# Optimization experiments

Hardware: AMD Instinct MI355X
Metric: run time of the kernel (lower is better)

## Reference

```python
import jax, jax.numpy as jnp
import numpy as np

TOKENS, IN_F, OUT_F = 16384, 4096, 4096
Q_MAX_I8 = 127.0


def setup_inputs() -> dict:
    key = jax.random.key(0)
    k1, k2, k3, k4 = jax.random.split(key, 4)
    x = jax.random.normal(k1, (TOKENS, IN_F), dtype=jnp.float32)
    # packed int4 weights: two nibbles per byte along dim=1 -> [out, in//2]
    qweight = jax.random.randint(k2, (OUT_F, IN_F // 2), 0, 256, dtype=jnp.int32)
    # per-output-channel symmetric scale (positive)
    weight_scale = jax.random.uniform(k3, (OUT_F, 1), dtype=jnp.float32) * 0.01 + 1e-4
    bias = jax.random.normal(k4, (OUT_F,), dtype=jnp.float32)
    return {"x": x, "qweight": qweight, "weight_scale": weight_scale, "bias": bias}


def _unpack_int4(qweight):
    # high nibble -> even columns, low nibble -> odd columns (pack dim=1)
    high = (qweight >> 4) - 8            # [out, in//2], values in [-8, 7]
    low = (qweight & 15) - 8
    out_f = qweight.shape[0]
    return jnp.stack([high, low], axis=-1).reshape(out_f, -1)  # [out, in]


def reference(x, qweight, weight_scale, bias):
    # dequantize int4 weight: per-output-channel symmetric scale
    w = _unpack_int4(qweight).astype(jnp.float32) * weight_scale  # [out, in]
    # dynamic per-sample symmetric int8 activation fake-quant
    max_abs = jnp.max(jnp.abs(x), axis=-1, keepdims=True)         # [tokens, 1]
    act_scale = max_abs / Q_MAX_I8
    act_scale = jnp.where(act_scale == 0, 1.0, act_scale)
    q_x = jnp.clip(jnp.round(x / act_scale), -128.0, 127.0)
    x_dq = q_x * act_scale
    return x_dq @ w.T + bias
```

## Files before the change

### kernel.cpp

```cpp
#include <hip/hip_runtime.h>
#include <cstdint>

#define TOKENS 16384
#define IN_F   4096
#define OUT_F  4096

typedef int v4i __attribute__((ext_vector_type(4)));

__device__ __forceinline__ void async_lds16(const void* g, const void* l) {
    __builtin_amdgcn_global_load_lds(
        (const __attribute__((address_space(1))) void*)(uintptr_t)g,
        (__attribute__((address_space(3))) void*)(uint32_t)(uintptr_t)l,
        16, 0, 0);
}

__global__ __launch_bounds__(256) void act_quant_kernel(
        const float* __restrict__ x,
        signed char* __restrict__ qx,
        float* __restrict__ act_scale) {
    const int row = blockIdx.x;
    const int tid = threadIdx.x;
    const float4* xr = (const float4*)(x + (size_t)row * IN_F);

    float4 v[4];
    float m = 0.f;
#pragma unroll
    for (int i = 0; i < 4; ++i) {
        v[i] = xr[i * 256 + tid];
        m = fmaxf(m, fmaxf(fmaxf(fabsf(v[i].x), fabsf(v[i].y)),
                           fmaxf(fabsf(v[i].z), fabsf(v[i].w))));
    }
#pragma unroll
    for (int off = 32; off > 0; off >>= 1)
        m = fmaxf(m, __shfl_xor(m, off, 64));
    __shared__ float wmax[4];
    if ((tid & 63) == 0) wmax[tid >> 6] = m;
    __syncthreads();
    m = fmaxf(fmaxf(wmax[0], wmax[1]), fmaxf(wmax[2], wmax[3]));

    const float inv = (m == 0.f) ? 0.f : 127.0f / m;
    if (tid == 0) act_scale[row] = (m == 0.f) ? 1.0f : m / 127.0f;

    int* qr = (int*)(qx + (size_t)row * IN_F);
#pragma unroll
    for (int i = 0; i < 4; ++i) {
        int q0 = (int)fminf(fmaxf(rintf(v[i].x * inv), -128.f), 127.f);
        int q1 = (int)fminf(fmaxf(rintf(v[i].y * inv), -128.f), 127.f);
        int q2 = (int)fminf(fmaxf(rintf(v[i].z * inv), -128.f), 127.f);
        int q3 = (int)fminf(fmaxf(rintf(v[i].w * inv), -128.f), 127.f);
        qr[i * 256 + tid] = (q0 & 255) | ((q1 & 255) << 8) |
                            ((q2 & 255) << 16) | ((q3 & 255) << 24);
    }
}

__global__ __launch_bounds__(256) void unpack_w_kernel(
        const int* __restrict__ qw,
        signed char* __restrict__ w8) {
    const size_t idx = ((size_t)blockIdx.x * 256 + threadIdx.x) * 4;
    const int4 q = *(const int4*)(qw + idx);
    const int b0 = ((((q.x >> 4) & 15) - 8) & 255);
    const int b1 = (((q.x & 15) - 8) & 255);
    const int b2 = ((((q.y >> 4) & 15) - 8) & 255);
    const int b3 = (((q.y & 15) - 8) & 255);
    const int b4 = ((((q.z >> 4) & 15) - 8) & 255);
    const int b5 = (((q.z & 15) - 8) & 255);
    const int b6 = ((((q.w >> 4) & 15) - 8) & 255);
    const int b7 = (((q.w & 15) - 8) & 255);
    int2 d;
    d.x = b0 | (b1 << 8) | (b2 << 16) | (b3 << 24);
    d.y = b4 | (b5 << 8) | (b6 << 16) | (b7 << 24);
    *(int2*)(w8 + idx * 2) = d;
}

__global__ __launch_bounds__(256, 2) void gemm_i8_kernel(
        const signed char* __restrict__ qx,
        const signed char* __restrict__ w8,
        const float* __restrict__ act_scale,
        const float* __restrict__ wscale,
        const float* __restrict__ bias,
        float* __restrict__ out) {
    __shared__ __align__(16) signed char sA[2][128 * 64];
    __shared__ __align__(16) signed char sB[2][256 * 64];

    const int nt = blockIdx.x & 15;
    const int mt = blockIdx.x >> 4;
    const int m0 = mt * 128, n0 = nt * 256;
    const int tid  = threadIdx.x;
    const int lane = tid & 63;
    const int wave = tid >> 6;
    const int wm = (wave >> 1) * 64;
    const int wn = (wave & 1) * 128;

    const int lrow = lane & 15;
    const int lcol = (lane >> 4) * 16;
    const signed char* gA0 = qx + (size_t)(m0 + 16 * (2 * wave) + lrow) * IN_F + lcol;
    const signed char* gA1 = gA0 + 16 * IN_F;
    const signed char* gB0 = w8 + (size_t)(n0 + 16 * (4 * wave) + lrow) * IN_F + lcol;
    const signed char* gB1 = gB0 + 16 * IN_F;
    const signed char* gB2 = gB0 + 32 * IN_F;
    const signed char* gB3 = gB0 + 48 * IN_F;
    const int aoff = (2 * wave) * 1024;
    const int boff = (4 * wave) * 1024;

    v4i acc[4][8];
#pragma unroll
    for (int i = 0; i < 4; ++i)
#pragma unroll
        for (int j = 0; j < 8; ++j) acc[i][j] = (v4i){0, 0, 0, 0};

    auto STAGE = [&](int buf, int k0) {
        signed char* a = sA[buf] + aoff;
        signed char* b = sB[buf] + boff;
        async_lds16(gA0 + k0, a);
        async_lds16(gA1 + k0, a + 1024);
        async_lds16(gB0 + k0, b);
        async_lds16(gB1 + k0, b + 1024);
        async_lds16(gB2 + k0, b + 2048);
        async_lds16(gB3 + k0, b + 3072);
    };

    auto COMPUTE = [&](int buf) {
        const signed char* fA = sA[buf] + (wm >> 4) * 1024 + lane * 16;
        const signed char* fB = sB[buf] + (wn >> 4) * 1024 + lane * 16;
        v4i af[4], bf[8];
#pragma unroll
        for (int i = 0; i < 4; ++i)
            af[i] = *(const v4i*)(fA + i * 1024);
#pragma unroll
        for (int j = 0; j < 8; ++j)
            bf[j] = *(const v4i*)(fB + j * 1024);
#pragma unroll
        for (int i = 0; i < 4; ++i)
#pragma unroll
            for (int j = 0; j < 8; ++j)
                acc[i][j] = __builtin_amdgcn_mfma_i32_16x16x64_i8(
                    af[i], bf[j], acc[i][j], 0, 0, 0);
    };

    STAGE(0, 0);
    int cur = 0;
    for (int k0 = 0; k0 < IN_F - 64; k0 += 64) {
        STAGE(cur ^ 1, k0 + 64);
        asm volatile("s_waitcnt vmcnt(6)" ::: "memory");
        __builtin_amdgcn_s_barrier();
        __builtin_amdgcn_sched_barrier(0);
        COMPUTE(cur);
        __builtin_amdgcn_sched_barrier(0);
        __builtin_amdgcn_s_barrier();
        cur ^= 1;
    }
    asm volatile("s_waitcnt vmcnt(0)" ::: "memory");
    __builtin_amdgcn_s_barrier();
    __builtin_amdgcn_sched_barrier(0);
    COMPUTE(cur);

    const int col_lane = lane & 15;
    const int row_q    = (lane >> 4) * 4;
    float4 as4[4];
#pragma unroll
    for (int i = 0; i < 4; ++i)
        as4[i] = *(const float4*)(act_scale + m0 + wm + i * 16 + row_q);

#pragma unroll
    for (int j = 0; j < 8; ++j) {
        const int n = n0 + wn + j * 16 + col_lane;
        const float wsn = wscale[n];
        const float bn  = bias[n];
#pragma unroll
        for (int i = 0; i < 4; ++i) {
            const int mb = m0 + wm + i * 16 + row_q;
            float* orow = out + (size_t)mb * OUT_F + n;
            const float* asp = (const float*)&as4[i];
#pragma unroll
            for (int r = 0; r < 4; ++r)
                orow[(size_t)r * OUT_F] = (float)acc[i][j][r] * (asp[r] * wsn) + bn;
        }
    }
}

extern "C" void kernel_launch(void* const* d_in, const int* in_sizes, int n_in,
                              void* d_out, int out_size, void* d_ws, size_t ws_size,
                              hipStream_t stream) {
    const float* x    = (const float*)d_in[0];
    const int*   qw   = (const int*)d_in[1];
    const float* wsc  = (const float*)d_in[2];
    const float* bias = (const float*)d_in[3];
    float* out = (float*)d_out;

    char* ws = (char*)d_ws;
    float*       act_scale = (float*)ws;
    signed char* qx        = (signed char*)(ws + 65536);
    signed char* w8        = (signed char*)(ws + 65536 + (size_t)TOKENS * IN_F);

    act_quant_kernel<<<TOKENS, 256, 0, stream>>>(x, qx, act_scale);
    unpack_w_kernel<<<(OUT_F * (IN_F / 2) / 4) / 256, 256, 0, stream>>>(qw, w8);
    gemm_i8_kernel<<<(TOKENS / 128) * (OUT_F / 256), 256, 0, stream>>>(
        qx, w8, act_scale, wsc, bias, out);
}
```

Baseline: 831.5 us.

## Keep weights packed int4 in GEMM, unpack in registers, fold zero-point via rowsums

Weights are repacked into a compact int4 byte layout rather than expanded to int8, and the GEMM unpacks nibbles in registers with masks. The -8 offset is handled by subtracting 8 times a per-row activation sum in the epilogue. Activations are interleaved at quantization time and loaded straight from global memory into registers instead of staged through LDS. The intent is to cut weight bandwidth and LDS traffic, at the cost of extra ALU unpack work per MFMA and non-LDS global A loads that may stall or coalesce poorly.

```diff
diff --git a/kernel.cpp b/kernel.cpp
--- a/kernel.cpp
+++ b/kernel.cpp
@@ -6,6 +6,7 @@
 #define OUT_F  4096
 
 typedef int v4i __attribute__((ext_vector_type(4)));
+typedef int v2i __attribute__((ext_vector_type(2)));
 
 __device__ __forceinline__ void async_lds16(const void* g, const void* l) {
     __builtin_amdgcn_global_load_lds(
@@ -17,7 +18,8 @@
 __global__ __launch_bounds__(256) void act_quant_kernel(
         const float* __restrict__ x,
         signed char* __restrict__ qx,
-        float* __restrict__ act_scale) {
+        float* __restrict__ act_scale,
+        int* __restrict__ rowsum) {
     const int row = blockIdx.x;
     const int tid = threadIdx.x;
     const float4* xr = (const float4*)(x + (size_t)row * IN_F);
@@ -34,6 +36,7 @@
     for (int off = 32; off > 0; off >>= 1)
         m = fmaxf(m, __shfl_xor(m, off, 64));
     __shared__ float wmax[4];
+    __shared__ int   wsum[4];
     if ((tid & 63) == 0) wmax[tid >> 6] = m;
     __syncthreads();
     m = fmaxf(fmaxf(wmax[0], wmax[1]), fmaxf(wmax[2], wmax[3]));
@@ -41,46 +44,58 @@
     const float inv = (m == 0.f) ? 0.f : 127.0f / m;
     if (tid == 0) act_scale[row] = (m == 0.f) ? 1.0f : m / 127.0f;
 
-    int* qr = (int*)(qx + (size_t)row * IN_F);
+    unsigned* qr = (unsigned*)(qx + (size_t)row * IN_F);
+    const int s = tid & 3;
+    const int dwpos = (s == 0) ? 0 : (s == 1) ? 2 : (s == 2) ? 1 : 3;
+    int lane_sum = 0;
 #pragma unroll
     for (int i = 0; i < 4; ++i) {
         int q0 = (int)fminf(fmaxf(rintf(v[i].x * inv), -128.f), 127.f);
         int q1 = (int)fminf(fmaxf(rintf(v[i].y * inv), -128.f), 127.f);
         int q2 = (int)fminf(fmaxf(rintf(v[i].z * inv), -128.f), 127.f);
         int q3 = (int)fminf(fmaxf(rintf(v[i].w * inv), -128.f), 127.f);
-        qr[i * 256 + tid] = (q0 & 255) | ((q1 & 255) << 8) |
-                            ((q2 & 255) << 16) | ((q3 & 255) << 24);
-    }
-}
-
-__global__ __launch_bounds__(256) void unpack_w_kernel(
+        lane_sum += q0 + q1 + q2 + q3;
+        unsigned D = (q0 & 255) | ((q1 & 255) << 8) |
+                     ((q2 & 255) << 16) | ((q3 & 255) << 24);
+        unsigned P = (unsigned)__shfl_xor((int)D, 1, 64);
+        unsigned Mo = ((s & 1) == 0)
+                    ? __builtin_amdgcn_perm(P, D, 0x07050301u)
+                    : __builtin_amdgcn_perm(D, P, 0x06040200u);
+        qr[i * 256 + (tid >> 2) * 4 + dwpos] = Mo;
+    }
+#pragma unroll
+    for (int off = 32; off > 0; off >>= 1)
+        lane_sum += __shfl_xor(lane_sum, off, 64);
+    if ((tid & 63) == 0) wsum[tid >> 6] = lane_sum;
+    __syncthreads();
+    if (tid == 0) rowsum[row] = wsum[0] + wsum[1] + wsum[2] + wsum[3];
+}
+
+__global__ __launch_bounds__(256) void repack_w_kernel(
         const int* __restrict__ qw,
-        signed char* __restrict__ w8) {
-    const size_t idx = ((size_t)blockIdx.x * 256 + threadIdx.x) * 4;
-    const int4 q = *(const int4*)(qw + idx);
-    const int b0 = ((((q.x >> 4) & 15) - 8) & 255);
-    const int b1 = (((q.x & 15) - 8) & 255);
-    const int b2 = ((((q.y >> 4) & 15) - 8) & 255);
-    const int b3 = (((q.y & 15) - 8) & 255);
-    const int b4 = ((((q.z >> 4) & 15) - 8) & 255);
-    const int b5 = (((q.z & 15) - 8) & 255);
-    const int b6 = ((((q.w >> 4) & 15) - 8) & 255);
-    const int b7 = (((q.w & 15) - 8) & 255);
-    int2 d;
-    d.x = b0 | (b1 << 8) | (b2 << 16) | (b3 << 24);
-    d.y = b4 | (b5 << 8) | (b6 << 16) | (b7 << 24);
-    *(int2*)(w8 + idx * 2) = d;
+        unsigned char* __restrict__ w4) {
+    const size_t idx = ((size_t)blockIdx.x * 256 + threadIdx.x) * 16;
+    const int4 a = *(const int4*)(qw + idx);
+    const int4 b = *(const int4*)(qw + idx + 4);
+    const int4 c = *(const int4*)(qw + idx + 8);
+    const int4 d = *(const int4*)(qw + idx + 12);
+    int4 o;
+    o.x = (a.x & 255) | ((a.y & 255) << 8) | ((a.z & 255) << 16) | (a.w << 24);
+    o.y = (b.x & 255) | ((b.y & 255) << 8) | ((b.z & 255) << 16) | (b.w << 24);
+    o.z = (c.x & 255) | ((c.y & 255) << 8) | ((c.z & 255) << 16) | (c.w << 24);
+    o.w = (d.x & 255) | ((d.y & 255) << 8) | ((d.z & 255) << 16) | (d.w << 24);
+    *(int4*)(w4 + idx) = o;
 }
 
 __global__ __launch_bounds__(256, 2) void gemm_i8_kernel(
         const signed char* __restrict__ qx,
-        const signed char* __restrict__ w8,
+        const unsigned char* __restrict__ w4,
         const float* __restrict__ act_scale,
+        const int* __restrict__ rowsum,
         const float* __restrict__ wscale,
         const float* __restrict__ bias,
         float* __restrict__ out) {
-    __shared__ __align__(16) signed char sA[2][128 * 64];
-    __shared__ __align__(16) signed char sB[2][256 * 64];
+    __shared__ __align__(16) unsigned char sB[2][8192];
 
     const int nt = blockIdx.x & 15;
     const int mt = blockIdx.x >> 4;
@@ -90,17 +105,16 @@
     const int wave = tid >> 6;
     const int wm = (wave >> 1) * 64;
     const int wn = (wave & 1) * 128;
-
     const int lrow = lane & 15;
-    const int lcol = (lane >> 4) * 16;
-    const signed char* gA0 = qx + (size_t)(m0 + 16 * (2 * wave) + lrow) * IN_F + lcol;
-    const signed char* gA1 = gA0 + 16 * IN_F;
-    const signed char* gB0 = w8 + (size_t)(n0 + 16 * (4 * wave) + lrow) * IN_F + lcol;
-    const signed char* gB1 = gB0 + 16 * IN_F;
-    const signed char* gB2 = gB0 + 32 * IN_F;
-    const signed char* gB3 = gB0 + 48 * IN_F;
-    const int aoff = (2 * wave) * 1024;
-    const int boff = (4 * wave) * 1024;
+    const int kc   = lane >> 4;
+
+    const signed char* aBase = qx + (size_t)(m0 + wm + lrow) * IN_F + kc * 16;
+
+    const unsigned char* bBase = w4 +
+        (size_t)(n0 + 64 * wave + 16 * (lane >> 5) + lrow) * (IN_F / 2) +
+        ((lane >> 4) & 1) * 16;
+
+    const int fOff = (wn >> 4) * 512 + lrow * 16 + (kc >> 1) * 256 + (kc & 1) * 8;
 
     v4i acc[4][8];
 #pragma unroll
@@ -109,57 +123,76 @@
         for (int j = 0; j < 8; ++j) acc[i][j] = (v4i){0, 0, 0, 0};
 
     auto STAGE = [&](int buf, int k0) {
-        signed char* a = sA[buf] + aoff;
-        signed char* b = sB[buf] + boff;
-        async_lds16(gA0 + k0, a);
-        async_lds16(gA1 + k0, a + 1024);
-        async_lds16(gB0 + k0, b);
-        async_lds16(gB1 + k0, b + 1024);
-        async_lds16(gB2 + k0, b + 2048);
-        async_lds16(gB3 + k0, b + 3072);
+        unsigned char* db = sB[buf] + 2 * wave * 1024;
+        async_lds16(bBase + (k0 >> 1), db);
+        async_lds16(bBase + (size_t)32 * (IN_F / 2) + (k0 >> 1), db + 1024);
     };
 
-    auto COMPUTE = [&](int buf) {
-        const signed char* fA = sA[buf] + (wm >> 4) * 1024 + lane * 16;
-        const signed char* fB = sB[buf] + (wn >> 4) * 1024 + lane * 16;
-        v4i af[4], bf[8];
-#pragma unroll
-        for (int i = 0; i < 4; ++i)
-            af[i] = *(const v4i*)(fA + i * 1024);
+#define LOADA(af, k0)                                                   \
+    {                                                                   \
+        _Pragma("unroll")                                               \
+        for (int i = 0; i < 4; ++i)                                     \
+            af[i] = *(const v4i*)(aBase + (size_t)i * 16 * IN_F + (k0)); \
+    }
+
+    auto COMPUTE = [&](int buf, const v4i* af) {
+        const unsigned char* fB = sB[buf] + fOff;
+        v2i pk[8];
 #pragma unroll
         for (int j = 0; j < 8; ++j)
-            bf[j] = *(const v4i*)(fB + j * 1024);
-#pragma unroll
-        for (int i = 0; i < 4; ++i)
-#pragma unroll
-            for (int j = 0; j < 8; ++j)
+            pk[j] = *(const v2i*)(fB + j * 512);
+#pragma unroll
+        for (int j = 0; j < 8; ++j) {
+            const unsigned ux = (unsigned)pk[j][0];
+            const unsigned uy = (unsigned)pk[j][1];
+            v4i bf;
+            bf[0] = (int)(ux & 0x0F0F0F0Fu);
+            bf[1] = (int)(uy & 0x0F0F0F0Fu);
+            bf[2] = (int)((ux >> 4) & 0x0F0F0F0Fu);
+            bf[3] = (int)((uy >> 4) & 0x0F0F0F0Fu);
+#pragma unroll
+            for (int i = 0; i < 4; ++i)
                 acc[i][j] = __builtin_amdgcn_mfma_i32_16x16x64_i8(
-                    af[i], bf[j], acc[i][j], 0, 0, 0);
+                    af[i], bf, acc[i][j], 0, 0, 0);
+        }
     };
 
+    v4i afA[4], afB[4];
+    LOADA(afA, 0);
     STAGE(0, 0);
-    int cur = 0;
-    for (int k0 = 0; k0 < IN_F - 64; k0 += 64) {
-        STAGE(cur ^ 1, k0 + 64);
+    for (int t = 0; t < 64; t += 2) {
+        const int k0 = t * 64;
+        LOADA(afB, k0 + 64);
+        STAGE(1, k0 + 64);
         asm volatile("s_waitcnt vmcnt(6)" ::: "memory");
         __builtin_amdgcn_s_barrier();
         __builtin_amdgcn_sched_barrier(0);
-        COMPUTE(cur);
-        __builtin_amdgcn_sched_barrier(0);
-        __builtin_amdgcn_s_barrier();
-        cur ^= 1;
-    }
-    asm volatile("s_waitcnt vmcnt(0)" ::: "memory");
-    __builtin_amdgcn_s_barrier();
-    __builtin_amdgcn_sched_barrier(0);
-    COMPUTE(cur);
+        COMPUTE(0, afA);
+        __builtin_amdgcn_sched_barrier(0);
+        __builtin_amdgcn_s_barrier();
+        if (t + 2 < 64) {
+            LOADA(afA, k0 + 128);
+            STAGE(0, k0 + 128);
+            asm volatile("s_waitcnt vmcnt(6)" ::: "memory");
+        } else {
+            asm volatile("s_waitcnt vmcnt(0)" ::: "memory");
+        }
+        __builtin_amdgcn_s_barrier();
+        __builtin_amdgcn_sched_barrier(0);
+        COMPUTE(1, afB);
+        __builtin_amdgcn_sched_barrier(0);
+        __builtin_amdgcn_s_barrier();
+    }
 
     const int col_lane = lane & 15;
     const int row_q    = (lane >> 4) * 4;
     float4 as4[4];
-#pragma unroll
-    for (int i = 0; i < 4; ++i)
+    int4   rs4[4];
+#pragma unroll
+    for (int i = 0; i < 4; ++i) {
         as4[i] = *(const float4*)(act_scale + m0 + wm + i * 16 + row_q);
+        rs4[i] = *(const int4*)(rowsum + m0 + wm + i * 16 + row_q);
+    }
 
 #pragma unroll
     for (int j = 0; j < 8; ++j) {
@@ -171,9 +204,11 @@
             const int mb = m0 + wm + i * 16 + row_q;
             float* orow = out + (size_t)mb * OUT_F + n;
             const float* asp = (const float*)&as4[i];
+            const int*   rsp = (const int*)&rs4[i];
 #pragma unroll
             for (int r = 0; r < 4; ++r)
-                orow[(size_t)r * OUT_F] = (float)acc[i][j][r] * (asp[r] * wsn) + bn;
+                orow[(size_t)r * OUT_F] =
+                    (float)(acc[i][j][r] - 8 * rsp[r]) * (asp[r] * wsn) + bn;
         }
     }
 }
@@ -188,12 +223,13 @@
     float* out = (float*)d_out;
 
     char* ws = (char*)d_ws;
-    float*       act_scale = (float*)ws;
-    signed char* qx        = (signed char*)(ws + 65536);
-    signed char* w8        = (signed char*)(ws + 65536 + (size_t)TOKENS * IN_F);
-
-    act_quant_kernel<<<TOKENS, 256, 0, stream>>>(x, qx, act_scale);
-    unpack_w_kernel<<<(OUT_F * (IN_F / 2) / 4) / 256, 256, 0, stream>>>(qw, w8);
+    float*         act_scale = (float*)ws;
+    int*           rowsum    = (int*)(ws + 65536);
+    signed char*   qx        = (signed char*)(ws + 131072);
+    unsigned char* w4        = (unsigned char*)(ws + 131072 + (size_t)TOKENS * IN_F);
+
+    act_quant_kernel<<<TOKENS, 256, 0, stream>>>(x, qx, act_scale, rowsum);
+    repack_w_kernel<<<(OUT_F * (IN_F / 2) / 16) / 256, 256, 0, stream>>>(qw, w4);
     gemm_i8_kernel<<<(TOKENS / 128) * (OUT_F / 256), 256, 0, stream>>>(
-        qx, w8, act_scale, wsc, bias, out);
-}
+        qx, w4, act_scale, rowsum, wsc, bias, out);
+}
```

Result: slower. 858.8 us (+3.3%).
